# Optimization experiments

Hardware: AMD Instinct MI355X
Metric: run time of the kernel (lower is better)

The kernel has to match this reference:

```python
import jax, jax.numpy as jnp
import numpy as np

DIM = 256; HEADS = 4; HD = DIM // HEADS; SCALE = HD ** -0.5
CBS = 4; CSTRIDE = 2; SBS = 4; NSEL = 16; WS = 7
B = 4; H = 64; W = 64


def _unfold(x, bs, stride):
    # x: (B,H,W,C) -> (B, nh*nw, C*bs*bs), flat channel order matches torch F.unfold
    # (index = c*bs*bs + kh*bs + kw)
    b, h, w, c = x.shape
    nh = (h - bs) // stride + 1
    nw = (w - bs) // stride + 1
    cols = [x[:, kh:kh + nh * stride:stride, kw:kw + nw * stride:stride, :]
            for kh in range(bs) for kw in range(bs)]
    p = jnp.stack(cols, axis=-1)  # (B,nh,nw,C,bs*bs)
    return p.reshape(b, nh * nw, c * bs * bs)


def _rel_pos_index(ws):
    coords = np.stack(np.meshgrid(np.arange(ws), np.arange(ws), indexing='ij')).reshape(2, -1)
    rel = (coords[:, :, None] - coords[:, None, :]).transpose(1, 2, 0).copy()
    rel[:, :, 0] += ws - 1
    rel[:, :, 1] += ws - 1
    rel[:, :, 0] *= 2 * ws - 1
    return jnp.asarray(rel.sum(-1))  # (ws*ws, ws*ws) int


def _mlp(x, w1, b1, w2, b2):
    return jax.nn.gelu(x @ w1 + b1, approximate=False) @ w2 + b2


def _window_attn(x, qkv_w, qkv_b, proj_w, proj_b, bias_table):
    b, c, h, w = x.shape
    ws = WS
    ph = (ws - h % ws) % ws
    pw = (ws - w % ws) % ws
    xp = jnp.pad(x, ((0, 0), (0, 0), (0, ph), (0, pw)))
    hp, wp = h + ph, w + pw
    xw = xp.reshape(b, c, hp // ws, ws, wp // ws, ws).transpose(0, 2, 4, 3, 5, 1).reshape(-1, ws * ws, c)
    bw = xw.shape[0]
    qkv = (xw @ qkv_w + qkv_b).reshape(bw, ws * ws, 3, HEADS, HD).transpose(2, 0, 3, 1, 4)
    q, k, v = qkv[0], qkv[1], qkv[2]
    attn = jnp.einsum('bhnd,bhmd->bhnm', q, k) * SCALE
    rpi = _rel_pos_index(ws)
    bias = bias_table[rpi.reshape(-1)].reshape(ws * ws, ws * ws, HEADS).transpose(2, 0, 1)
    attn = jax.nn.softmax(attn + bias[None], axis=-1)
    o = jnp.einsum('bhnm,bhmd->bhnd', attn, v).transpose(0, 2, 1, 3).reshape(bw, ws * ws, c)
    o = o @ proj_w + proj_b
    o = o.reshape(b, hp // ws, wp // ws, ws, ws, c).transpose(0, 5, 1, 3, 2, 4).reshape(b, c, hp, wp)
    return o[:, :, :h, :w]


def _forward(x, qkv_cmp_w, qkv_cmp_b, qkv_slc_w, qkv_slc_b,
             cmpk_w1, cmpk_b1, cmpk_w2, cmpk_b2,
             cmpv_w1, cmpv_b1, cmpv_w2, cmpv_b2, pos_embed,
             win_qkv_w, win_qkv_b, win_proj_w, win_proj_b, win_bias_table,
             proj_cmp_w, proj_cmp_b, proj_slc_w, proj_slc_b,
             gate_w1, gate_b1, gate_w2, gate_b2):
    b, c, h, w = x.shape
    n = h * w
    xs = x.reshape(b, c, n).transpose(0, 2, 1)  # (B,N,C)

    # --- compressed branch ---
    qkv = (xs @ qkv_cmp_w + qkv_cmp_b).reshape(b, n, 3, HEADS, HD).transpose(2, 0, 3, 1, 4)
    q_c, k_c, v_c = qkv[0], qkv[1], qkv[2]  # (B,heads,N,hd)
    k_flat = k_c.transpose(0, 2, 1, 3).reshape(b, n, c)
    v_flat = v_c.transpose(0, 2, 1, 3).reshape(b, n, c)
    fk = _unfold(k_flat.reshape(b, h, w, c), CBS, CSTRIDE)  # (B,nb,C*16)
    fv = _unfold(v_flat.reshape(b, h, w, c), CBS, CSTRIDE)
    nb = fk.shape[1]
    # replicate torch's reshape of the channel-major unfold vector into (bs*bs, dim)
    kpos = (fk.reshape(b, nb, CBS * CBS, c) + pos_embed[None]).reshape(b, nb, CBS * CBS * c)
    k_cmp = _mlp(kpos, cmpk_w1, cmpk_b1, cmpk_w2, cmpk_b2)  # (B,nb,C)
    v_cmp = _mlp(fv, cmpv_w1, cmpv_b1, cmpv_w2, cmpv_b2)
    kch = k_cmp.reshape(b, nb, HEADS, HD).transpose(0, 2, 1, 3)
    vch = v_cmp.reshape(b, nb, HEADS, HD).transpose(0, 2, 1, 3)
    attn_cmp = jax.nn.softmax(jnp.einsum('bhnd,bhmd->bhnm', q_c, kch) * SCALE, axis=-1)
    out_cmp = jnp.einsum('bhnm,bhmd->bhnd', attn_cmp, vch).transpose(0, 2, 1, 3).reshape(b, n, c)
    out_cmp = out_cmp @ proj_cmp_w + proj_cmp_b

    # --- selected branch ---
    qkv2 = (xs @ qkv_slc_w + qkv_slc_b).reshape(b, n, 3, HEADS, HD).transpose(2, 0, 3, 1, 4)
    q_s, k_s, v_s = qkv2[0], qkv2[1], qkv2[2]
    ks_flat = k_s.transpose(0, 2, 1, 3).reshape(b, n, c)
    vs_flat = v_s.transpose(0, 2, 1, 3).reshape(b, n, c)
    imp = attn_cmp.sum(axis=1).mean(axis=1)  # (B, nb)
    ns = min(NSEL, nb)
    _, idx = jax.lax.top_k(imp, ns)
    fkb = _unfold(ks_flat.reshape(b, h, w, c), SBS, SBS)
    fvb = _unfold(vs_flat.reshape(b, h, w, c), SBS, SBS)
    nb2 = fkb.shape[1]
    kb = fkb.reshape(b, nb2, SBS * SBS, c)
    vb = fvb.reshape(b, nb2, SBS * SBS, c)
    idx = jnp.clip(idx, 0, nb2 - 1)
    k_slc = jnp.take_along_axis(kb, idx[:, :, None, None], axis=1).reshape(b, ns * SBS * SBS, c)
    v_slc = jnp.take_along_axis(vb, idx[:, :, None, None], axis=1).reshape(b, ns * SBS * SBS, c)
    ksh = k_slc.reshape(b, -1, HEADS, HD).transpose(0, 2, 1, 3)
    vsh = v_slc.reshape(b, -1, HEADS, HD).transpose(0, 2, 1, 3)
    attn_slc = jax.nn.softmax(jnp.einsum('bhnd,bhmd->bhnm', q_s, ksh) * SCALE, axis=-1)
    out_slc = jnp.einsum('bhnm,bhmd->bhnd', attn_slc, vsh).transpose(0, 2, 1, 3).reshape(b, n, c)
    out_slc = out_slc @ proj_slc_w + proj_slc_b

    # --- window branch ---
    out_win = _window_attn(x, win_qkv_w, win_qkv_b, win_proj_w, win_proj_b, win_bias_table)
    out_win = out_win.reshape(b, c, n).transpose(0, 2, 1)

    # --- gated combination ---
    g = jax.nn.sigmoid(jax.nn.gelu(xs @ gate_w1 + gate_b1, approximate=False) @ gate_w2 + gate_b2)
    out = g[..., 0:1] * out_cmp + g[..., 1:2] * out_slc + g[..., 2:3] * out_win
    return out.transpose(0, 2, 1).reshape(b, c, h, w)


def setup_inputs() -> dict:
    key = jax.random.key(0)
    ks = jax.random.split(key, 16)
    s = 0.02
    d = {
        'x': jax.random.normal(ks[0], (B, DIM, H, W), jnp.float32),
        'qkv_cmp_w': jax.random.normal(ks[1], (DIM, 3 * DIM)) * s,
        'qkv_cmp_b': jnp.zeros((3 * DIM,)),
        'qkv_slc_w': jax.random.normal(ks[2], (DIM, 3 * DIM)) * s,
        'qkv_slc_b': jnp.zeros((3 * DIM,)),
        'cmpk_w1': jax.random.normal(ks[3], (DIM * CBS * CBS, 2 * DIM)) * s,
        'cmpk_b1': jnp.zeros((2 * DIM,)),
        'cmpk_w2': jax.random.normal(ks[4], (2 * DIM, DIM)) * s,
        'cmpk_b2': jnp.zeros((DIM,)),
        'cmpv_w1': jax.random.normal(ks[5], (DIM * CBS * CBS, 2 * DIM)) * s,
        'cmpv_b1': jnp.zeros((2 * DIM,)),
        'cmpv_w2': jax.random.normal(ks[6], (2 * DIM, DIM)) * s,
        'cmpv_b2': jnp.zeros((DIM,)),
        'pos_embed': jax.random.normal(ks[7], (1, CBS * CBS, DIM)) * s,
        'win_qkv_w': jax.random.normal(ks[8], (DIM, 3 * DIM)) * s,
        'win_qkv_b': jnp.zeros((3 * DIM,)),
        'win_proj_w': jax.random.normal(ks[9], (DIM, DIM)) * s,
        'win_proj_b': jnp.zeros((DIM,)),
        'win_bias_table': jax.random.normal(ks[10], ((2 * WS - 1) ** 2, HEADS)) * s,
        'proj_cmp_w': jax.random.normal(ks[11], (DIM, DIM)) * s,
        'proj_cmp_b': jnp.zeros((DIM,)),
        'proj_slc_w': jax.random.normal(ks[12], (DIM, DIM)) * s,
        'proj_slc_b': jnp.zeros((DIM,)),
        'gate_w1': jax.random.normal(ks[13], (DIM, DIM // 4)) * s,
        'gate_b1': jnp.zeros((DIM // 4,)),
        'gate_w2': jax.random.normal(ks[14], (DIM // 4, 3)) * s,
        'gate_b2': jnp.zeros((3,)),
    }
    return d


def reference(x, qkv_cmp_w, qkv_cmp_b, qkv_slc_w, qkv_slc_b,
              cmpk_w1, cmpk_b1, cmpk_w2, cmpk_b2,
              cmpv_w1, cmpv_b1, cmpv_w2, cmpv_b2, pos_embed,
              win_qkv_w, win_qkv_b, win_proj_w, win_proj_b, win_bias_table,
              proj_cmp_w, proj_cmp_b, proj_slc_w, proj_slc_b,
              gate_w1, gate_b1, gate_w2, gate_b2):
    return _forward(x, qkv_cmp_w, qkv_cmp_b, qkv_slc_w, qkv_slc_b,
                    cmpk_w1, cmpk_b1, cmpk_w2, cmpk_b2,
                    cmpv_w1, cmpv_b1, cmpv_w2, cmpv_b2, pos_embed,
                    win_qkv_w, win_qkv_b, win_proj_w, win_proj_b, win_bias_table,
                    proj_cmp_w, proj_cmp_b, proj_slc_w, proj_slc_b,
                    gate_w1, gate_b1, gate_w2, gate_b2)
```

## Files before the change

kernel.cpp:

```cpp
#include <hip/hip_runtime.h>
#include <stdint.h>
#include <stddef.h>


#define DEV __device__ __forceinline__

typedef __attribute__((ext_vector_type(8))) short short8;
typedef __attribute__((ext_vector_type(4))) float f32x4;
typedef unsigned short u16;

DEV u16 f2bf(float f){
    unsigned u = __float_as_uint(f);
    u += 0x7FFFu + ((u>>16)&1u);
    return (u16)(u>>16);
}
DEV float bf2f(u16 u){ return __uint_as_float(((unsigned)u)<<16); }

#define LGKM0() asm volatile("s_waitcnt lgkmcnt(0)" ::: "memory")

__global__ void k_xs(const float* __restrict__ x, u16* __restrict__ xh,
                     u16* __restrict__ xl){
    __shared__ float t[32][33];
    int b = blockIdx.z; int c0 = blockIdx.y*32; int n0 = blockIdx.x*32;
    int tx = threadIdx.x, ty = threadIdx.y;
    for(int i=ty;i<32;i+=8)
        t[i][tx] = x[((size_t)(b*256 + c0+i))*4096 + n0 + tx];
    __syncthreads();
    for(int i=ty;i<32;i+=8){
        float v = t[tx][i];
        u16 h = f2bf(v);
        size_t o = ((size_t)(b*4096 + n0+i))*256 + c0 + tx;
        xh[o] = h;
        xl[o] = f2bf(v - bf2f(h));
    }
}

__global__ void k_wt(const float* __restrict__ W, u16* __restrict__ WT,
                     int K, int N){
    __shared__ float t[32][33];
    int k0 = blockIdx.x*32, n0 = blockIdx.y*32;
    int tx = threadIdx.x, ty = threadIdx.y;
    for(int i=ty;i<32;i+=8)
        if(k0+i<K && n0+tx<N) t[i][tx] = W[(size_t)(k0+i)*N + n0+tx];
    __syncthreads();
    for(int i=ty;i<32;i+=8)
        if(n0+i<N && k0+tx<K) WT[(size_t)(n0+i)*K + k0+tx] = f2bf(t[tx][i]);
}

__global__ void k_wt2(const float* __restrict__ W, u16* __restrict__ Hi,
                      u16* __restrict__ Lo, int K, int N){
    __shared__ float t[32][33];
    int k0 = blockIdx.x*32, n0 = blockIdx.y*32;
    int tx = threadIdx.x, ty = threadIdx.y;
    for(int i=ty;i<32;i+=8)
        if(k0+i<K && n0+tx<N) t[i][tx] = W[(size_t)(k0+i)*N + n0+tx];
    __syncthreads();
    for(int i=ty;i<32;i+=8)
        if(n0+i<N && k0+tx<K){
            float v = t[tx][i];
            u16 h = f2bf(v);
            Hi[(size_t)(n0+i)*K + k0+tx] = h;
            Lo[(size_t)(n0+i)*K + k0+tx] = f2bf(v - bf2f(h));
        }
}

__global__ void k_vt(const float* __restrict__ vc, u16* __restrict__ vt,
                     int NK, int ldk){
    __shared__ float t[32][33];
    int b = blockIdx.z; int k0 = blockIdx.x*32; int c0 = blockIdx.y*32;
    int tx = threadIdx.x, ty = threadIdx.y;
    for(int i=ty;i<32;i+=8){
        int k = k0+i;
        t[i][tx] = (k < NK) ? vc[((size_t)(b*NK + k))*256 + c0 + tx] : 0.f;
    }
    __syncthreads();
    for(int i=ty;i<32;i+=8){
        int k = k0+tx;
        if(k < ldk)
            vt[((size_t)(b*256 + c0+i))*ldk + k] = f2bf(t[tx][i]);
    }
}

__global__ __launch_bounds__(256) void k_gemm(
        const float* __restrict__ A, const float* __restrict__ W,
        const float* __restrict__ bias, float* __restrict__ C,
        int M, int K, int Nn, int act)
{
    __shared__ float As[16][68];
    __shared__ float Bs[16][64];
    const int m0 = blockIdx.y*64, n0 = blockIdx.x*64;
    const int t = threadIdx.x, tx = t&15, ty = t>>4;
    float acc[4][4] = {};
    const int am = t>>2;
    const int ak = (t&3)*4;
    const bool arow_ok = (m0+am) < M;

    for(int k0=0;k0<K;k0+=16){
        float4 av = make_float4(0.f,0.f,0.f,0.f);
        if(arow_ok) av = *reinterpret_cast<const float4*>(&A[(size_t)(m0+am)*K + k0 + ak]);
        As[ak+0][am]=av.x; As[ak+1][am]=av.y; As[ak+2][am]=av.z; As[ak+3][am]=av.w;
        {
            int n = t&63, kb = t>>6;
            #pragma unroll
            for(int r=0;r<4;r++){
                int kk = r*4 + kb; float v = 0.f;
                if(n0+n < Nn) v = W[(size_t)(k0+kk)*Nn + n0+n];
                Bs[kk][n] = v;
            }
        }
        __syncthreads();
        #pragma unroll
        for(int kk=0;kk<16;kk++){
            float a0=As[kk][ty*4+0], a1=As[kk][ty*4+1], a2=As[kk][ty*4+2], a3=As[kk][ty*4+3];
            float b0=Bs[kk][tx*4+0], b1=Bs[kk][tx*4+1], b2=Bs[kk][tx*4+2], b3=Bs[kk][tx*4+3];
            acc[0][0]=fmaf(a0,b0,acc[0][0]); acc[0][1]=fmaf(a0,b1,acc[0][1]);
            acc[0][2]=fmaf(a0,b2,acc[0][2]); acc[0][3]=fmaf(a0,b3,acc[0][3]);
            acc[1][0]=fmaf(a1,b0,acc[1][0]); acc[1][1]=fmaf(a1,b1,acc[1][1]);
            acc[1][2]=fmaf(a1,b2,acc[1][2]); acc[1][3]=fmaf(a1,b3,acc[1][3]);
            acc[2][0]=fmaf(a2,b0,acc[2][0]); acc[2][1]=fmaf(a2,b1,acc[2][1]);
            acc[2][2]=fmaf(a2,b2,acc[2][2]); acc[2][3]=fmaf(a2,b3,acc[2][3]);
            acc[3][0]=fmaf(a3,b0,acc[3][0]); acc[3][1]=fmaf(a3,b1,acc[3][1]);
            acc[3][2]=fmaf(a3,b2,acc[3][2]); acc[3][3]=fmaf(a3,b3,acc[3][3]);
        }
        __syncthreads();
    }
    #pragma unroll
    for(int i=0;i<4;i++){
        int m = m0 + ty*4 + i;
        if(m >= M) continue;
        #pragma unroll
        for(int j=0;j<4;j++){
            int n = n0 + tx*4 + j;
            if(n >= Nn) continue;
            float v = acc[i][j] + (bias ? bias[n] : 0.f);
            if(act==1)      v = 0.5f*v*(1.0f + erff(v*0.70710678118654752f));
            else if(act==2) v = 1.0f/(1.0f + expf(-v));
            C[(size_t)m*Nn + n] = v;
        }
    }
}

template<int WM, int WN, int AM, int BMD, int NSPLIT, int OBF>
__global__ __launch_bounds__(256) void k_mgs(
        const float* __restrict__ Af, const u16* __restrict__ Ah,
        const u16* __restrict__ Al,
        const float* __restrict__ Bf, const u16* __restrict__ Bh,
// ... 87 lines not shown
                        h[j] = (short)hb;
                        if(SP) l[j] = (short)f2bf(vv[j] - bf2f(hb));
                    }
                } else {
                    if(lok){
                        h = *reinterpret_cast<const short8*>(Bh + (size_t)(n0+brow)*ldb + kt + e);
                        if(SP && BMD==2)
                            l = *reinterpret_cast<const short8*>(Bl + (size_t)(n0+brow)*ldb + kt + e);
                    }
                }
                int byteoff = brow*128 + (colbyte ^ ((brow&7)<<4));
                *reinterpret_cast<short8*>(reinterpret_cast<char*>(Bhi)+byteoff) = h;
                if(SP)
                    *reinterpret_cast<short8*>(reinterpret_cast<char*>(Blo)+byteoff) = l;
            }
        }
        __syncthreads();
        __builtin_amdgcn_s_setprio(1);
        #pragma unroll
        for(int kb=0;kb<2;kb++){
            short8 ah[WM], al[WM], bh[WN], bl[WN];
            #pragma unroll
            for(int i=0;i<WM;i++){
                int ar = wm + i*16 + (lane&15);
                int ab = ar*128 + (((kb*64) + ((lane>>4)*16)) ^ ((ar&7)<<4));
                ah[i] = *reinterpret_cast<const short8*>(reinterpret_cast<const char*>(Ahi)+ab);
                if(SP)
                    al[i] = *reinterpret_cast<const short8*>(reinterpret_cast<const char*>(Alo)+ab);
            }
            #pragma unroll
            for(int i=0;i<WN;i++){
                int br = wn + i*16 + (lane&15);
                int bb = br*128 + (((kb*64) + ((lane>>4)*16)) ^ ((br&7)<<4));
                bh[i] = *reinterpret_cast<const short8*>(reinterpret_cast<const char*>(Bhi)+bb);
                if(SP)
                    bl[i] = *reinterpret_cast<const short8*>(reinterpret_cast<const char*>(Blo)+bb);
            }
            #pragma unroll
            for(int mi=0;mi<WM;mi++)
                #pragma unroll
                for(int ni=0;ni<WN;ni++){
                    if(SP){
                        acc[mi][ni] = __builtin_amdgcn_mfma_f32_16x16x32_bf16(
                                          al[mi], bh[ni], acc[mi][ni], 0, 0, 0);
                        acc[mi][ni] = __builtin_amdgcn_mfma_f32_16x16x32_bf16(
                                          ah[mi], bl[ni], acc[mi][ni], 0, 0, 0);
                    }
                    acc[mi][ni] = __builtin_amdgcn_mfma_f32_16x16x32_bf16(
                                      ah[mi], bh[ni], acc[mi][ni], 0, 0, 0);
                }
        }
        __builtin_amdgcn_s_setprio(0);
        __syncthreads();
    }
    #pragma unroll
    for(int mi=0;mi<WM;mi++){
        #pragma unroll
        for(int ni=0;ni<WN;ni++){
            int col = n0 + wn + ni*16 + (lane&15);
            if(col >= N) continue;
            int rowb = m0 + wm + mi*16 + ((lane>>4)*4);
            float bv = bias ? bias[col] : 0.f;
            #pragma unroll
            for(int r=0;r<4;r++){
                int m = rowb + r;
                if(m >= M) continue;
                float v = acc[mi][ni][r]*scale + bv;
                if(act==1)      v = 0.5f*v*(1.0f + erff(v*0.70710678118654752f));
                else if(act==2) v = 1.0f/(1.0f + expf(-v));
                if(OBF==2){
                    u16 hb = f2bf(v);
                    Cb [(size_t)m*ldc + col] = hb;
                    Cb2[(size_t)m*ldc + col] = f2bf(v - bf2f(hb));
                } else if(OBF==1){
                    Cb[(size_t)m*ldc + col] = f2bf(v);
                } else {
                    C [(size_t)m*ldc + col] = v;
                }
            }
        }
    }
}

template<int SPLIT, int IMP, int ONEPASS, int NKR, int NT, int LDV>
__global__ __launch_bounds__(256) void k_fattn(
    const float* __restrict__ Qg, const u16* __restrict__ Khg,
    const u16* __restrict__ Klg, const u16* __restrict__ VTg,
    u16* __restrict__ Og, float* __restrict__ impp)
{
    const int qb = blockIdx.x, h = blockIdx.y, b = blockIdx.z;
    const int tid = threadIdx.x, lane = tid&63, wv = tid>>6;
    const int wm = wv*16;
    const int rgrp = lane>>4;
    const int cidx = lane&15;

    __shared__ u16 Qh[64*64];
    __shared__ u16 Ql[SPLIT?64*64:8];
    __shared__ u16 Kh[64*64];
    __shared__ u16 Kl[SPLIT?64*64:8];
    __shared__ u16 Pl[64*64];
    __shared__ u16 Vl[64*64];
    __shared__ float part[4][64];
    __shared__ float colacc[IMP? NT*64 : 8];

    const int srow = tid>>2;
    const int scol0 = (tid&3)*32;

    short8 kh_r[2], kl_r[2], v_r[2];

    auto LK = [&](int t){
        const bool ok = (t*64 + srow) < NKR;
        const u16* srch = &Khg[((size_t)b*NKR + t*64 + srow)*256 + h*64];
        const u16* srcl = SPLIT ? &Klg[((size_t)b*NKR + t*64 + srow)*256 + h*64] : nullptr;
        #pragma unroll
        for(int c=0;c<2;c++){
            int e = (scol0 + c*16)>>1;
            short8 hh = {}, ll = {};
            if(ok){
                hh = *reinterpret_cast<const short8*>(srch+e);
                if(SPLIT) ll = *reinterpret_cast<const short8*>(srcl+e);
            }
            kh_r[c] = hh;
            if(SPLIT) kl_r[c] = ll;
        }
    };
    auto WK = [&](){
        #pragma unroll
        for(int c=0;c<2;c++){
            int colbyte = scol0 + c*16;
            int byteoff = srow*128 + (colbyte ^ ((srow&7)<<4));
            *reinterpret_cast<short8*>(reinterpret_cast<char*>(Kh)+byteoff) = kh_r[c];
            if(SPLIT)
                *reinterpret_cast<short8*>(reinterpret_cast<char*>(Kl)+byteoff) = kl_r[c];
        }
    };
    auto LV = [&](int t){
        const u16* src = &VTg[((size_t)b*256 + h*64 + srow)*LDV + t*64];
        #pragma unroll
        for(int c=0;c<2;c++){
            int e = (scol0 + c*16)>>1;
            short8 hh = {};
            if(t*64 + e + 8 <= LDV)
                hh = *reinterpret_cast<const short8*>(src + e);
            v_r[c] = hh;
        }
    };
    auto WV = [&](){
        #pragma unroll
        for(int c=0;c<2;c++){
            int colbyte = scol0 + c*16;
            int byteoff = srow*128 + (colbyte ^ ((srow&7)<<4));
            *reinterpret_cast<short8*>(reinterpret_cast<char*>(Vl)+byteoff) = v_r[c];
        }
    };

    {
        const float* src = &Qg[((size_t)b*4096 + qb*64 + srow)*768 + h*64];
        #pragma unroll
        for(int c=0;c<2;c++){
            int colbyte = scol0 + c*16;
            int e = colbyte>>1;
            float4 v0 = *reinterpret_cast<const float4*>(src+e);
            float4 v1 = *reinterpret_cast<const float4*>(src+e+4);
            float vv[8]={v0.x,v0.y,v0.z,v0.w,v1.x,v1.y,v1.z,v1.w};
            short8 hh, ll;
            #pragma unroll
// ... 96 lines not shown
                    acc[ni] = __builtin_amdgcn_mfma_f32_16x16x32_bf16(ah, bl, acc[ni], 0,0,0);
                }
                acc[ni] = __builtin_amdgcn_mfma_f32_16x16x32_bf16(ah, bh, acc[ni], 0,0,0);
            }
        }
        __builtin_amdgcn_s_setprio(0);
        float cs[4] = {0.f,0.f,0.f,0.f};
        #pragma unroll
        for(int ni=0;ni<4;ni++){
            #pragma unroll
            for(int r=0;r<4;r++){
                int col = kt + ni*16 + cidx;
                float p = 0.f;
                if(col < NKR){
                    p = __expf(acc[ni][r]*0.125f);
                    if(!ONEPASS) p *= inv[r];
                    else lsum[r] += p;
                }
                int prow = wm + rgrp*4 + r;
                int pcol = ni*16 + cidx;
                int byteoff = prow*128 + ((pcol*2) ^ ((prow&7)<<4));
                *reinterpret_cast<u16*>(reinterpret_cast<char*>(Pl)+byteoff) = f2bf(p);
                if(IMP) cs[ni] += p;
            }
        }
        if(IMP){
            #pragma unroll
            for(int ni=0;ni<4;ni++){
                cs[ni] += __shfl_xor(cs[ni],16);
                cs[ni] += __shfl_xor(cs[ni],32);
            }
            if(rgrp==0){
                #pragma unroll
                for(int ni=0;ni<4;ni++)
                    part[wv][ni*16+cidx] = cs[ni];
            }
        }
        LGKM0();
        __builtin_amdgcn_s_barrier();
        if(IMP && tid < 64)
            colacc[kt+tid] += ((part[0][tid]+part[1][tid])+part[2][tid])+part[3][tid];
        __builtin_amdgcn_s_setprio(1);
        #pragma unroll
        for(int kb=0;kb<2;kb++){
            int koff = kb*64 + rgrp*16;
            int ar = wm + cidx;
            int ab = ar*128 + (koff ^ ((ar&7)<<4));
            short8 pa = *reinterpret_cast<const short8*>(reinterpret_cast<const char*>(Pl)+ab);
            #pragma unroll
            for(int ni=0;ni<4;ni++){
                int br = ni*16 + cidx;
                int bb = br*128 + (koff ^ ((br&7)<<4));
                short8 vb = *reinterpret_cast<const short8*>(reinterpret_cast<const char*>(Vl)+bb);
                acc_o[ni] = __builtin_amdgcn_mfma_f32_16x16x32_bf16(pa, vb, acc_o[ni], 0,0,0);
            }
        }
        __builtin_amdgcn_s_setprio(0);
    }
    if(ONEPASS){
        #pragma unroll
        for(int r=0;r<4;r++){
            float l = lsum[r];
            l += __shfl_xor(l,1); l += __shfl_xor(l,2);
            l += __shfl_xor(l,4); l += __shfl_xor(l,8);
            inv[r] = 1.f/l;
        }
    }
    __syncthreads();
    #pragma unroll
    for(int ni=0;ni<4;ni++){
        #pragma unroll
        for(int r=0;r<4;r++){
            int q = qb*64 + wm + rgrp*4 + r;
            int d = ni*16 + cidx;
            float o = acc_o[ni][r];
            if(ONEPASS) o *= inv[r];
            Og[((size_t)b*4096 + q)*256 + h*64 + d] = f2bf(o);
        }
    }
    if(IMP){
        size_t base = ((size_t)((b*4+h)*64) + qb)*976;
        for(int k=tid; k<NT*64 && k<976; k+=256)
            impp[base+k] = colacc[k];
    }
}

__global__ void k_unfold2(const float* __restrict__ qkv, const float* __restrict__ pos,
                          u16* __restrict__ kh, u16* __restrict__ kl,
                          u16* __restrict__ vv){
    int row = blockIdx.x;
    int b = row / 961, blk = row % 961;
    int bi = blk / 31, bj = blk % 31;
    for(int j = threadIdx.x; j < 4096; j += 256){
        int ch = j >> 4;
        int khh = (j >> 2) & 3, kw = j & 3;
        int n = (bi*2 + khh)*64 + (bj*2 + kw);
        size_t base = ((size_t)(b*4096) + n)*768 + ch;
        float kv = qkv[base + 256] + pos[j];
        float va = qkv[base + 512];
        u16 h = f2bf(kv);
        kh[(size_t)row*4096 + j] = h;
        kl[(size_t)row*4096 + j] = f2bf(kv - bf2f(h));
        vv[(size_t)row*4096 + j] = f2bf(va);
    }
}

__global__ void k_imp_reduce(const float* __restrict__ impp, float* __restrict__ imp){
    __shared__ float part[4][64];
    int b = blockIdx.y;
    int k = blockIdx.x*64 + (threadIdx.x & 63);
    int rr = threadIdx.x >> 6;
    float s = 0.f;
    if(k < 976){
        for(int r=rr; r<256; r+=4)
            s += impp[((size_t)(b*256) + r)*976 + k];
    }
    part[rr][threadIdx.x & 63] = s;
    __syncthreads();
    if(threadIdx.x < 64 && k < 961){
        float t = ((part[0][threadIdx.x] + part[1][threadIdx.x])
                 + part[2][threadIdx.x]) + part[3][threadIdx.x];
        imp[b*961 + k] = t;
    }
}

__global__ __launch_bounds__(256) void k_topk(const float* __restrict__ imp,
                                              int* __restrict__ idx){
    int b = blockIdx.x;
    __shared__ float v[961];
    __shared__ float wvv[4];
    __shared__ int   wvi[4];
    int t = threadIdx.x;
    int lane = t & 63, wid = t >> 6;
    for(int i=t;i<961;i+=256) v[i] = imp[b*961+i];
    __syncthreads();
    for(int it=0; it<16; it++){
        float bv = -1e30f; int bi = 1<<30;
        for(int i=t;i<961;i+=256){
            float val = v[i];
            if(val > bv){ bv=val; bi=i; }
        }
        #pragma unroll
        for(int off=32; off>0; off>>=1){
            float ov = __shfl_xor(bv, off);
            int   oi = __shfl_xor(bi, off);
            if(ov > bv || (ov == bv && oi < bi)){ bv = ov; bi = oi; }
        }
        if(lane==0){ wvv[wid]=bv; wvi[wid]=bi; }
        __syncthreads();
        if(t==0){
            float gb=wvv[0]; int gi=wvi[0];
            #pragma unroll
            for(int w=1;w<4;w++){
                if(wvv[w]>gb || (wvv[w]==gb && wvi[w]<gi)){ gb=wvv[w]; gi=wvi[w]; }
            }
            idx[b*16+it] = gi;
            v[gi] = -1e30f;
        }
        __syncthreads();
    }
}

__global__ void k_gather_sel(const float* __restrict__ qkv2, const int* __restrict__ idx,
                             u16* __restrict__ Ks, float* __restrict__ Vs){
    int row = blockIdx.x;
    int b = row >> 8, tt = row & 255;
    int sel = tt >> 4, p = tt & 15;
    int blk = idx[b*16+sel]; if(blk > 255) blk = 255;
    int bi = blk >> 4, bj = blk & 15;
    int cc = threadIdx.x;
    int y = bi*4 + ((cc>>2)&3), xx = bj*4 + (cc&3);
    int ch = p*16 + (cc>>4);
    size_t src = ((size_t)(b*4096) + y*64 + xx)*768;
    Ks[(size_t)row*256 + cc] = f2bf(qkv2[src + 256 + ch]);
    Vs[(size_t)row*256 + cc] = qkv2[src + 512 + ch];
}

__global__ void k_xw(const u16* __restrict__ xh, u16* __restrict__ xw){
    int row = blockIdx.x;
    int wb = row / 49, t = row % 49;
    int b = wb / 100, wrem = wb % 100;
    int wy = wrem / 10, wx = wrem % 10;
    int ty = t / 7, tx = t % 7;
    int y = wy*7 + ty, xx = wx*7 + tx;
    int c = threadIdx.x;
    u16 v = 0;
// ... 45 lines not shown
        for(int d=0;d<64;d++){
            float a0=0,a1=0;
            for(int j=0;j<48;j+=2){
                a0 = fmaf(ls[lane][j],   lv[j][d],   a0);
                a1 = fmaf(ls[lane][j+1], lv[j+1][d], a1);
            }
            a0 = fmaf(ls[lane][48], lv[48][d], a0);
            op[d] = f2bf((a0+a1)*inv);
        }
    }
}

__global__ void k_combine(const float* __restrict__ ocp, const float* __restrict__ osp,
                          const float* __restrict__ owp, const float* __restrict__ g,
                          float* __restrict__ out){
    __shared__ float tile[32][33];
    int b = blockIdx.z; int c0 = blockIdx.y*32, n0 = blockIdx.x*32;
    int tx = threadIdx.x, ty = threadIdx.y;
    for(int i=ty;i<32;i+=8){
        int n = n0 + i;
        float g0 = g[(size_t)(b*4096+n)*3 + 0];
        float g1 = g[(size_t)(b*4096+n)*3 + 1];
        float g2 = g[(size_t)(b*4096+n)*3 + 2];
        int y = n >> 6, xx = n & 63;
        int wy = y/7, ty2 = y%7, wx = xx/7, tx2 = xx%7;
        size_t wrow = (size_t)(b*100 + wy*10 + wx)*49 + ty2*7 + tx2;
        size_t base = ((size_t)(b*4096) + n)*256 + c0;
        float vc = ocp[base + tx];
        float vs = osp[base + tx];
        float vw = owp[wrow*256 + c0 + tx];
        tile[i][tx] = g0*vc + g1*vs + g2*vw;
    }
    __syncthreads();
    for(int i=ty;i<32;i+=8)
        out[((size_t)(b*256 + c0+i))*4096 + n0 + tx] = tile[tx][i];
}

extern "C" void kernel_launch(void* const* d_in, const int* in_sizes, int n_in,
                              void* d_out, int out_size, void* d_ws, size_t ws_size,
                              hipStream_t stream)
{
    typedef const float* fp;
    fp x          = (fp)d_in[0];
    fp qkv_cmp_w  = (fp)d_in[1];  fp qkv_cmp_b = (fp)d_in[2];
    fp qkv_slc_w  = (fp)d_in[3];  fp qkv_slc_b = (fp)d_in[4];
    fp cmpk_w1    = (fp)d_in[5];  fp cmpk_b1   = (fp)d_in[6];
    fp cmpk_w2    = (fp)d_in[7];  fp cmpk_b2   = (fp)d_in[8];
    fp cmpv_w1    = (fp)d_in[9];  fp cmpv_b1   = (fp)d_in[10];
    fp cmpv_w2    = (fp)d_in[11]; fp cmpv_b2   = (fp)d_in[12];
    fp pos_embed  = (fp)d_in[13];
    fp win_qkv_w  = (fp)d_in[14]; fp win_qkv_b = (fp)d_in[15];
    fp win_proj_w = (fp)d_in[16]; fp win_proj_b= (fp)d_in[17];
    fp win_btab   = (fp)d_in[18];
    fp proj_cmp_w = (fp)d_in[19]; fp proj_cmp_b= (fp)d_in[20];
    fp proj_slc_w = (fp)d_in[21]; fp proj_slc_b= (fp)d_in[22];
    fp gate_w1    = (fp)d_in[23]; fp gate_b1   = (fp)d_in[24];
    fp gate_w2    = (fp)d_in[25]; fp gate_b2   = (fp)d_in[26];
    (void)in_sizes; (void)n_in; (void)out_size;

    char* ws = (char*)d_ws;
    size_t off = 0;
    auto alloc = [&](size_t bytes)->size_t{
        size_t r = off; off += (bytes + 255) & ~(size_t)255; return r;
    };
    const size_t XSH  = alloc((size_t)16384*256*2);
    const size_t XSL  = alloc((size_t)16384*256*2);
    const size_t QKV  = alloc((size_t)16384*768*4);
    const size_t BIGA = alloc((size_t)4*4096*976*4);
    const size_t HID  = alloc((size_t)3844*512*4);
    const size_t KCH  = alloc((size_t)3844*256*2);
    const size_t KCL  = alloc((size_t)3844*256*2);
    const size_t VC   = alloc((size_t)3844*256*4);
    const size_t S_IMPP = (size_t)4096*976*4;
    const size_t S_OC   = (size_t)16384*256*4;
    const size_t S_PB   = (size_t)4*4096*976*2;
    const size_t POOL = alloc(S_IMPP + S_OC + S_OC + S_PB);
    const size_t IMP  = alloc((size_t)4*961*4);
    const size_t IDX  = alloc((size_t)4*16*4);
    const size_t KS   = alloc((size_t)4*256*256*2);
    const size_t VS   = alloc((size_t)4*256*256*4);
    const size_t G2   = alloc((size_t)16384*3*4);
    const size_t VTC  = alloc((size_t)4*256*976*2);
    const size_t VTS  = alloc((size_t)4*256*256*2);
    const size_t TQS  = alloc((size_t)768*256*2);
    const size_t TWQ  = alloc((size_t)768*256*2);
    const size_t TV1  = alloc((size_t)512*4096*2);
    const size_t TV2  = alloc((size_t)256*512*2);
    const size_t TPC  = alloc((size_t)256*256*2);
    const size_t TPS  = alloc((size_t)256*256*2);
    const size_t TWP  = alloc((size_t)256*256*2);
    const size_t TG1  = alloc((size_t)64*256*2);
    const size_t TQCH = alloc((size_t)768*256*2);
    const size_t TQCL = alloc((size_t)768*256*2);
    const size_t TK1H = alloc((size_t)512*4096*2);
    const size_t TK1L = alloc((size_t)512*4096*2);
    const size_t TK2H = alloc((size_t)256*512*2);
    const size_t TK2L = alloc((size_t)256*512*2);
    if(off > ws_size) return;

    u16*   p_xsh = (u16*)(ws + XSH);
    u16*   p_xsl = (u16*)(ws + XSL);
    float* p_qkv = (float*)(ws + QKV);
    u16*   p_bigb= (u16*)  (ws + BIGA);
    u16*   p_uv  = (u16*)  (ws + BIGA);
    float* p_oslc= (float*)(ws + BIGA);
    float* p_owp = (float*)(ws + BIGA + 20971520);
    float* p_hid = (float*)(ws + HID);
    u16*   p_kch = (u16*)(ws + KCH);
    u16*   p_kcl = (u16*)(ws + KCL);
    float* p_vc  = (float*)(ws + VC);
    float* p_impp= (float*)(ws + POOL);
    u16*   p_oc16= (u16*)  (ws + POOL + S_IMPP);
    float* p_ocp = (float*)(ws + POOL + S_IMPP + S_OC);
    u16*   p_ukh = (u16*)  (ws + POOL);
    u16*   p_ukl = p_ukh + (size_t)3844*4096;
    u16*   p_xwb = (u16*)  (ws + POOL);
    u16*   p_owin= (u16*)  (ws + POOL + S_IMPP);
    float* p_imp = (float*)(ws + IMP);
    int*   p_idx = (int*)  (ws + IDX);
    u16*   p_ks  = (u16*)(ws + KS);
    float* p_vs  = (float*)(ws + VS);
    float* p_g   = (float*)(ws + G2);
    u16*   p_vtc = (u16*)(ws + VTC);
    u16*   p_vts = (u16*)(ws + VTS);
    u16* t_qs = (u16*)(ws + TQS);
    u16* t_wq = (u16*)(ws + TWQ);
    u16* t_v1 = (u16*)(ws + TV1);
    u16* t_v2 = (u16*)(ws + TV2);
    u16* t_pc = (u16*)(ws + TPC);
    u16* t_ps = (u16*)(ws + TPS);
    u16* t_wp = (u16*)(ws + TWP);
    u16* t_g1 = (u16*)(ws + TG1);
    u16* t_qch= (u16*)(ws + TQCH);
    u16* t_qcl= (u16*)(ws + TQCL);
    u16* t_k1h= (u16*)(ws + TK1H);
    u16* t_k1l= (u16*)(ws + TK1L);
    u16* t_k2h= (u16*)(ws + TK2H);
    u16* t_k2l= (u16*)(ws + TK2L);

    auto wt = [&](fp W, u16* WT, int K, int Nn){
        k_wt<<<dim3((K+31)/32, (Nn+31)/32), dim3(32,8), 0, stream>>>(W, WT, K, Nn);
    };
    auto wt2 = [&](fp W, u16* H, u16* L, int K, int Nn){
        k_wt2<<<dim3((K+31)/32, (Nn+31)/32), dim3(32,8), 0, stream>>>(W, H, L, K, Nn);
    };

    wt(qkv_slc_w, t_qs, 256, 768);
    wt(win_qkv_w, t_wq, 256, 768);
    wt(cmpv_w1,   t_v1, 4096, 512);
    wt(cmpv_w2,   t_v2, 512, 256);
    wt(proj_cmp_w,t_pc, 256, 256);
    wt(proj_slc_w,t_ps, 256, 256);
    wt(win_proj_w,t_wp, 256, 256);
    wt(gate_w1,   t_g1, 256, 64);
    wt2(qkv_cmp_w, t_qch, t_qcl, 256, 768);
    wt2(cmpk_w1,   t_k1h, t_k1l, 4096, 512);
    wt2(cmpk_w2,   t_k2h, t_k2l, 512, 256);

    k_xs<<<dim3(128,8,4), dim3(32,8), 0, stream>>>(x, p_xsh, p_xsl);
    k_mgs<4,4,2,2,3,0><<<dim3(6,128), 256, 0, stream>>>(
        nullptr, p_xsh, p_xsl, nullptr, t_qch, t_qcl, qkv_cmp_b, p_qkv, nullptr, nullptr,
        16384, 768, 256, 256, 256, 768, 0, 1.0f, 0, 0, 0);
    k_unfold2<<<3844, 256, 0, stream>>>(p_qkv, pos_embed, p_ukh, p_ukl, p_uv);
    k_mgs<2,2,2,2,3,0><<<dim3(8,61), 256, 0, stream>>>(
        nullptr, p_ukh, p_ukl, nullptr, t_k1h, t_k1l, cmpk_b1, p_hid, nullptr, nullptr,
        3844, 512, 4096, 4096, 4096, 512, 1, 1.0f, 0, 0, 0);
    k_mgs<2,2,0,2,3,2><<<dim3(4,61), 256, 0, stream>>>(
        p_hid, nullptr, nullptr, nullptr, t_k2h, t_k2l, cmpk_b2, nullptr, p_kch, p_kcl,
        3844, 256, 512, 512, 512, 256, 0, 1.0f, 0, 0, 0);
    k_mgs<2,2,1,1,1,0><<<dim3(8,61), 256, 0, stream>>>(
        nullptr, p_uv, nullptr, nullptr, t_v1, nullptr, cmpv_b1, p_hid, nullptr, nullptr,
        3844, 512, 4096, 4096, 4096, 512, 1, 1.0f, 0, 0, 0);
    k_mgs<2,2,0,1,1,0><<<dim3(4,61), 256, 0, stream>>>(
        p_hid, nullptr, nullptr, nullptr, t_v2, nullptr, cmpv_b2, p_vc, nullptr, nullptr,
        3844, 256, 512, 512, 512, 256, 0, 1.0f, 0, 0, 0);
    k_vt<<<dim3(31,8,4), dim3(32,8), 0, stream>>>(p_vc, p_vtc, 961, 976);
    k_fattn<1,1,0,961,16,976><<<dim3(64,4,4), 256, 0, stream>>>(
        p_qkv, p_kch, p_kcl, p_vtc, p_oc16, p_impp);
    k_imp_reduce<<<dim3(16,4), 256, 0, stream>>>(p_impp, p_imp);
    k_topk<<<4, 256, 0, stream>>>(p_imp, p_idx);
    k_mgs<4,4,1,1,1,0><<<dim3(2,128), 256, 0, stream>>>(
        nullptr, p_oc16, nullptr, nullptr, t_pc, nullptr, proj_cmp_b, p_ocp, nullptr, nullptr,
        16384, 256, 256, 256, 256, 256, 0, 1.0f, 0, 0, 0);
    k_mgs<4,4,1,1,1,0><<<dim3(6,128), 256, 0, stream>>>(
        nullptr, p_xsh, nullptr, nullptr, t_qs, nullptr, qkv_slc_b, p_qkv, nullptr, nullptr,
        16384, 768, 256, 256, 256, 768, 0, 1.0f, 0, 0, 0);
    k_xw<<<19600, 256, 0, stream>>>(p_xsh, p_xwb);
    k_mgs<4,4,1,1,1,1><<<dim3(6,154), 256, 0, stream>>>(
        nullptr, p_xwb, nullptr, nullptr, t_wq, nullptr, win_qkv_b, nullptr, p_bigb, nullptr,
        19600, 768, 256, 256, 256, 768, 0, 1.0f, 0, 0, 0);
    k_attn_win<<<dim3(400,4), 64, 0, stream>>>(p_bigb, win_btab, p_owin);
    k_mgs<4,4,1,1,1,0><<<dim3(2,154), 256, 0, stream>>>(
        nullptr, p_owin, nullptr, nullptr, t_wp, nullptr, win_proj_b, p_owp, nullptr, nullptr,
        19600, 256, 256, 256, 256, 256, 0, 1.0f, 0, 0, 0);
    k_gather_sel<<<1024, 256, 0, stream>>>(p_qkv, p_idx, p_ks, p_vs);
    k_vt<<<dim3(8,8,4), dim3(32,8), 0, stream>>>(p_vs, p_vts, 256, 256);
    k_fattn<0,0,1,256,4,256><<<dim3(64,4,4), 256, 0, stream>>>(
        p_qkv, p_ks, nullptr, p_vts, p_oc16, nullptr);
    k_mgs<4,4,1,1,1,0><<<dim3(2,128), 256, 0, stream>>>(
        nullptr, p_oc16, nullptr, nullptr, t_ps, nullptr, proj_slc_b, p_oslc, nullptr, nullptr,
        16384, 256, 256, 256, 256, 256, 0, 1.0f, 0, 0, 0);
    k_mgs<2,2,1,1,1,0><<<dim3(1,256), 256, 0, stream>>>(
        nullptr, p_xsh, nullptr, nullptr, t_g1, nullptr, gate_b1, p_hid, nullptr, nullptr,
        16384, 64, 256, 256, 256, 64, 1, 1.0f, 0, 0, 0);
    k_gemm<<<dim3(1,256), 256, 0, stream>>>(p_hid, gate_w2, gate_b2, p_g,
                                            16384, 64, 3, 2);
    k_combine<<<dim3(128,8,4), dim3(32,8), 0, stream>>>(p_ocp, p_oslc, p_owp, p_g,
                                                        (float*)d_out);
}
```

Before: 794.0 us.

## Fuse unfold into compressor GEMM loads and fold pos_embed into bias

Drops the materialized unfold buffers, which held about 3844x4096 hi/lo/v bf16 values. The compressor MLP GEMMs now gather their A tiles straight from per-token K/V arrays, using a permuted K ordering in the transposed weights so each 64-wide k-tile is one contiguous channel span of a single patch position. The pos_embed addition is moved into the first-layer bias as pos@W1+b1, computed once by a small kernel. This removes a large write-then-read of the unfolded data. In exchange the A loads are strided gathers, and pos_embed is no longer split into hi/lo parts inside the K path, which slightly changes the rounding.

```diff
diff --git a/kernel.cpp b/kernel.cpp
--- a/kernel.cpp
+++ b/kernel.cpp
@@ -36,19 +36,7 @@
 }
 
 __global__ void k_wt(const float* __restrict__ W, u16* __restrict__ WT,
-                     int K, int N){
-    __shared__ float t[32][33];
-    int k0 = blockIdx.x*32, n0 = blockIdx.y*32;
-    int tx = threadIdx.x, ty = threadIdx.y;
-    for(int i=ty;i<32;i+=8)
-        if(k0+i<K && n0+tx<N) t[i][tx] = W[(size_t)(k0+i)*N + n0+tx];
-    __syncthreads();
-    for(int i=ty;i<32;i+=8)
-        if(n0+i<N && k0+tx<K) WT[(size_t)(n0+i)*K + k0+tx] = f2bf(t[tx][i]);
-}
-
-__global__ void k_wt2(const float* __restrict__ W, u16* __restrict__ Hi,
-                      u16* __restrict__ Lo, int K, int N){
+                     int K, int N, int perm){
     __shared__ float t[32][33];
     int k0 = blockIdx.x*32, n0 = blockIdx.y*32;
     int tx = threadIdx.x, ty = threadIdx.y;
@@ -57,11 +45,55 @@
     __syncthreads();
     for(int i=ty;i<32;i+=8)
         if(n0+i<N && k0+tx<K){
+            int k = k0+tx;
+            int kd = perm ? (((k&15)<<8)|(k>>4)) : k;
+            WT[(size_t)(n0+i)*K + kd] = f2bf(t[tx][i]);
+        }
+}
+
+__global__ void k_wt2(const float* __restrict__ W, u16* __restrict__ Hi,
+                      u16* __restrict__ Lo, int K, int N, int perm){
+    __shared__ float t[32][33];
+    int k0 = blockIdx.x*32, n0 = blockIdx.y*32;
+    int tx = threadIdx.x, ty = threadIdx.y;
+    for(int i=ty;i<32;i+=8)
+        if(k0+i<K && n0+tx<N) t[i][tx] = W[(size_t)(k0+i)*N + n0+tx];
+    __syncthreads();
+    for(int i=ty;i<32;i+=8)
+        if(n0+i<N && k0+tx<K){
+            int k = k0+tx;
+            int kd = perm ? (((k&15)<<8)|(k>>4)) : k;
             float v = t[tx][i];
             u16 h = f2bf(v);
-            Hi[(size_t)(n0+i)*K + k0+tx] = h;
-            Lo[(size_t)(n0+i)*K + k0+tx] = f2bf(v - bf2f(h));
-        }
+            Hi[(size_t)(n0+i)*K + kd] = h;
+            Lo[(size_t)(n0+i)*K + kd] = f2bf(v - bf2f(h));
+        }
+}
+
+__global__ void k_splitkv(const float* __restrict__ qkv, u16* __restrict__ kh,
+                          u16* __restrict__ kl, u16* __restrict__ vf){
+    int n = blockIdx.x, b = blockIdx.y, c = threadIdx.x;
+    size_t src = ((size_t)(b*4096) + n)*768 + c;
+    size_t dst = ((size_t)(b*4096) + n)*256 + c;
+    float kv = qkv[src + 256];
+    u16 h = f2bf(kv);
+    kh[dst] = h;
+    kl[dst] = f2bf(kv - bf2f(h));
+    vf[dst] = f2bf(qkv[src + 512]);
+}
+
+__global__ void k_posw1(const float* __restrict__ pos, const float* __restrict__ W1,
+                        const float* __restrict__ b1, float* __restrict__ out){
+    __shared__ float part[4][64];
+    int tn = threadIdx.x & 63, r = threadIdx.x >> 6;
+    int n = blockIdx.x*64 + tn;
+    float s = 0.f;
+    for(int j=r; j<4096; j+=4)
+        s += pos[j] * W1[(size_t)j*512 + n];
+    part[r][tn] = s;
+    __syncthreads();
+    if(threadIdx.x < 64)
+        out[n] = b1[n] + (((part[0][tn]+part[1][tn])+part[2][tn])+part[3][tn]);
 }
 
 __global__ void k_vt(const float* __restrict__ vc, u16* __restrict__ vt,
@@ -315,6 +347,130 @@
     }
 }
 
+template<int SPLIT>
+__global__ __launch_bounds__(256) void k_mgs_unf(
+        const u16* __restrict__ Fh, const u16* __restrict__ Fl,
+        const u16* __restrict__ Bh, const u16* __restrict__ Bl,
+        const float* __restrict__ bias, float* __restrict__ C)
+{
+    constexpr int M = 3844, N = 512, K = 4096;
+    __shared__ u16 Ahi[64*64];
+    __shared__ u16 Alo[SPLIT ? 64*64 : 8];
+    __shared__ u16 Bhi[64*64];
+    __shared__ u16 Blo[SPLIT ? 64*64 : 8];
+
+    const int m0 = blockIdx.y*64, n0 = blockIdx.x*64;
+    const int tid = threadIdx.x, lane = tid&63, wv = tid>>6;
+    const int wm = (wv>>1)*32, wn = (wv&1)*32;
+    f32x4 acc[2][2] = {};
+
+    const int arow = tid >> 2;
+    const int acol0 = (tid & 3) * 32;
+    const int m = m0 + arow;
+    const bool ok = m < M;
+    const int mm = ok ? m : 0;
+    const int b  = mm / 961;
+    const int blk = mm % 961;
+    const int bi = blk / 31, bj = blk % 31;
+    const u16* fbase_h = Fh + (size_t)b*4096*256;
+    const u16* fbase_l = SPLIT ? (Fl + (size_t)b*4096*256) : nullptr;
+
+    for(int kt=0; kt<K; kt+=64){
+        {
+            int sub = kt >> 8;
+            int kh = sub >> 2, kw = sub & 3;
+            int n = (bi*2 + kh)*64 + (bj*2 + kw);
+            size_t srcoff = (size_t)n*256 + (kt & 255);
+            #pragma unroll
+            for(int c=0;c<2;c++){
+                int colbyte = acol0 + c*16;
+                int e = colbyte >> 1;
+                short8 h = {}, l = {};
+                if(ok){
+                    h = *reinterpret_cast<const short8*>(fbase_h + srcoff + e);
+                    if(SPLIT)
+                        l = *reinterpret_cast<const short8*>(fbase_l + srcoff + e);
+                }
+                int byteoff = arow*128 + (colbyte ^ ((arow&7)<<4));
+                *reinterpret_cast<short8*>(reinterpret_cast<char*>(Ahi)+byteoff) = h;
+                if(SPLIT)
+                    *reinterpret_cast<short8*>(reinterpret_cast<char*>(Alo)+byteoff) = l;
+            }
+        }
+        {
+            int brow = tid >> 2;
+            int bcol0 = (tid & 3) * 32;
+            #pragma unroll
+            for(int c=0;c<2;c++){
+                int colbyte = bcol0 + c*16;
+                int e = colbyte >> 1;
+                short8 h = *reinterpret_cast<const short8*>(Bh + (size_t)(n0+brow)*K + kt + e);
+                short8 l = {};
+                if(SPLIT)
+                    l = *reinterpret_cast<const short8*>(Bl + (size_t)(n0+brow)*K + kt + e);
+                int byteoff = brow*128 + (colbyte ^ ((brow&7)<<4));
+                *reinterpret_cast<short8*>(reinterpret_cast<char*>(Bhi)+byteoff) = h;
+                if(SPLIT)
+                    *reinterpret_cast<short8*>(reinterpret_cast<char*>(Blo)+byteoff) = l;
+            }
+        }
+        __syncthreads();
+        __builtin_amdgcn_s_setprio(1);
+        #pragma unroll
+        for(int kb=0;kb<2;kb++){
+            short8 ah[2], al[2], bh[2], bl[2];
+            #pragma unroll
+            for(int i=0;i<2;i++){
+                int ar = wm + i*16 + (lane&15);
+                int ab = ar*128 + (((kb*64) + ((lane>>4)*16)) ^ ((ar&7)<<4));
+                ah[i] = *reinterpret_cast<const short8*>(reinterpret_cast<const char*>(Ahi)+ab);
+                if(SPLIT)
+                    al[i] = *reinterpret_cast<const short8*>(reinterpret_cast<const char*>(Alo)+ab);
+            }
+            #pragma unroll
+            for(int i=0;i<2;i++){
+                int br = wn + i*16 + (lane&15);
+                int bb = br*128 + (((kb*64) + ((lane>>4)*16)) ^ ((br&7)<<4));
+                bh[i] = *reinterpret_cast<const short8*>(reinterpret_cast<const char*>(Bhi)+bb);
+                if(SPLIT)
+                    bl[i] = *reinterpret_cast<const short8*>(reinterpret_cast<const char*>(Blo)+bb);
+            }
+            #pragma unroll
+            for(int mi=0;mi<2;mi++)
+                #pragma unroll
+                for(int ni=0;ni<2;ni++){
+                    if(SPLIT){
+                        acc[mi][ni] = __builtin_amdgcn_mfma_f32_16x16x32_bf16(
+                                          al[mi], bh[ni], acc[mi][ni], 0, 0, 0);
+                        acc[mi][ni] = __builtin_amdgcn_mfma_f32_16x16x32_bf16(
+                                          ah[mi], bl[ni], acc[mi][ni], 0, 0, 0);
+                    }
+                    acc[mi][ni] = __builtin_amdgcn_mfma_f32_16x16x32_bf16(
+                                      ah[mi], bh[ni], acc[mi][ni], 0, 0, 0);
+                }
+        }
+        __builtin_amdgcn_s_setprio(0);
+        __syncthreads();
+    }
+    #pragma unroll
+    for(int mi=0;mi<2;mi++){
+        #pragma unroll
+        for(int ni=0;ni<2;ni++){
+            int col = n0 + wn + ni*16 + (lane&15);
+            int rowb = m0 + wm + mi*16 + ((lane>>4)*4);
+            float bv = bias[col];
+            #pragma unroll
+            for(int r=0;r<4;r++){
+                int mr = rowb + r;
+                if(mr >= M) continue;
+                float v = acc[mi][ni][r] + bv;
+                v = 0.5f*v*(1.0f + erff(v*0.70710678118654752f));
+                C[(size_t)mr*512 + col] = v;
+            }
+        }
+    }
+}
+
 template<int SPLIT, int IMP, int ONEPASS, int NKR, int NT, int LDV>
 __global__ __launch_bounds__(256) void k_fattn(
     const float* __restrict__ Qg, const u16* __restrict__ Khg,
@@ -577,26 +733,6 @@
         size_t base = ((size_t)((b*4+h)*64) + qb)*976;
         for(int k=tid; k<NT*64 && k<976; k+=256)
             impp[base+k] = colacc[k];
-    }
-}
-
-__global__ void k_unfold2(const float* __restrict__ qkv, const float* __restrict__ pos,
-                          u16* __restrict__ kh, u16* __restrict__ kl,
-                          u16* __restrict__ vv){
-    int row = blockIdx.x;
-    int b = row / 961, blk = row % 961;
-    int bi = blk / 31, bj = blk % 31;
-    for(int j = threadIdx.x; j < 4096; j += 256){
-        int ch = j >> 4;
-        int khh = (j >> 2) & 3, kw = j & 3;
-        int n = (bi*2 + khh)*64 + (bj*2 + kw);
-        size_t base = ((size_t)(b*4096) + n)*768 + ch;
-        float kv = qkv[base + 256] + pos[j];
-        float va = qkv[base + 512];
-        u16 h = f2bf(kv);
-        kh[(size_t)row*4096 + j] = h;
-        kl[(size_t)row*4096 + j] = f2bf(kv - bf2f(h));
-        vv[(size_t)row*4096 + j] = f2bf(va);
     }
 }
 
@@ -808,6 +944,7 @@
     const size_t G2   = alloc((size_t)16384*3*4);
     const size_t VTC  = alloc((size_t)4*256*976*2);
     const size_t VTS  = alloc((size_t)4*256*256*2);
+    const size_t POSB = alloc((size_t)512*4);
     const size_t TQS  = alloc((size_t)768*256*2);
     const size_t TWQ  = alloc((size_t)768*256*2);
     const size_t TV1  = alloc((size_t)512*4096*2);
@@ -828,7 +965,6 @@
     u16*   p_xsl = (u16*)(ws + XSL);
     float* p_qkv = (float*)(ws + QKV);
     u16*   p_bigb= (u16*)  (ws + BIGA);
-    u16*   p_uv  = (u16*)  (ws + BIGA);
     float* p_oslc= (float*)(ws + BIGA);
     float* p_owp = (float*)(ws + BIGA + 20971520);
     float* p_hid = (float*)(ws + HID);
@@ -838,8 +974,9 @@
     float* p_impp= (float*)(ws + POOL);
     u16*   p_oc16= (u16*)  (ws + POOL + S_IMPP);
     float* p_ocp = (float*)(ws + POOL + S_IMPP + S_OC);
-    u16*   p_ukh = (u16*)  (ws + POOL);
-    u16*   p_ukl = p_ukh + (size_t)3844*4096;
+    u16*   p_kfh = (u16*)  (ws + POOL);
+    u16*   p_kfl = p_kfh + (size_t)4*4096*256;
+    u16*   p_vf  = p_kfl + (size_t)4*4096*256;
     u16*   p_xwb = (u16*)  (ws + POOL);
     u16*   p_owin= (u16*)  (ws + POOL + S_IMPP);
     float* p_imp = (float*)(ws + IMP);
@@ -849,6 +986,7 @@
     float* p_g   = (float*)(ws + G2);
     u16*   p_vtc = (u16*)(ws + VTC);
     u16*   p_vts = (u16*)(ws + VTS);
+    float* p_posb= (float*)(ws + POSB);
     u16* t_qs = (u16*)(ws + TQS);
     u16* t_wq = (u16*)(ws + TWQ);
     u16* t_v1 = (u16*)(ws + TV1);
@@ -864,39 +1002,38 @@
     u16* t_k2h= (u16*)(ws + TK2H);
     u16* t_k2l= (u16*)(ws + TK2L);
 
-    auto wt = [&](fp W, u16* WT, int K, int Nn){
-        k_wt<<<dim3((K+31)/32, (Nn+31)/32), dim3(32,8), 0, stream>>>(W, WT, K, Nn);
+    auto wt = [&](fp W, u16* WT, int K, int Nn, int perm){
+        k_wt<<<dim3((K+31)/32, (Nn+31)/32), dim3(32,8), 0, stream>>>(W, WT, K, Nn, perm);
     };
-    auto wt2 = [&](fp W, u16* H, u16* L, int K, int Nn){
-        k_wt2<<<dim3((K+31)/32, (Nn+31)/32), dim3(32,8), 0, stream>>>(W, H, L, K, Nn);
+    auto wt2 = [&](fp W, u16* H, u16* L, int K, int Nn, int perm){
+        k_wt2<<<dim3((K+31)/32, (Nn+31)/32), dim3(32,8), 0, stream>>>(W, H, L, K, Nn, perm);
     };
 
-    wt(qkv_slc_w, t_qs, 256, 768);
-    wt(win_qkv_w, t_wq, 256, 768);
-    wt(cmpv_w1,   t_v1, 4096, 512);
-    wt(cmpv_w2,   t_v2, 512, 256);
-    wt(proj_cmp_w,t_pc, 256, 256);
-    wt(proj_slc_w,t_ps, 256, 256);
-    wt(win_proj_w,t_wp, 256, 256);
-    wt(gate_w1,   t_g1, 256, 64);
-    wt2(qkv_cmp_w, t_qch, t_qcl, 256, 768);
-    wt2(cmpk_w1,   t_k1h, t_k1l, 4096, 512);
-    wt2(cmpk_w2,   t_k2h, t_k2l, 512, 256);
+    wt(qkv_slc_w, t_qs, 256, 768, 0);
+    wt(win_qkv_w, t_wq, 256, 768, 0);
+    wt(cmpv_w1,   t_v1, 4096, 512, 1);
+    wt(cmpv_w2,   t_v2, 512, 256, 0);
+    wt(proj_cmp_w,t_pc, 256, 256, 0);
+    wt(proj_slc_w,t_ps, 256, 256, 0);
+    wt(win_proj_w,t_wp, 256, 256, 0);
+    wt(gate_w1,   t_g1, 256, 64, 0);
+    wt2(qkv_cmp_w, t_qch, t_qcl, 256, 768, 0);
+    wt2(cmpk_w1,   t_k1h, t_k1l, 4096, 512, 1);
+    wt2(cmpk_w2,   t_k2h, t_k2l, 512, 256, 0);
+    k_posw1<<<8, 256, 0, stream>>>(pos_embed, cmpk_w1, cmpk_b1, p_posb);
 
     k_xs<<<dim3(128,8,4), dim3(32,8), 0, stream>>>(x, p_xsh, p_xsl);
     k_mgs<4,4,2,2,3,0><<<dim3(6,128), 256, 0, stream>>>(
         nullptr, p_xsh, p_xsl, nullptr, t_qch, t_qcl, qkv_cmp_b, p_qkv, nullptr, nullptr,
         16384, 768, 256, 256, 256, 768, 0, 1.0f, 0, 0, 0);
-    k_unfold2<<<3844, 256, 0, stream>>>(p_qkv, pos_embed, p_ukh, p_ukl, p_uv);
-    k_mgs<2,2,2,2,3,0><<<dim3(8,61), 256, 0, stream>>>(
-        nullptr, p_ukh, p_ukl, nullptr, t_k1h, t_k1l, cmpk_b1, p_hid, nullptr, nullptr,
-        3844, 512, 4096, 4096, 4096, 512, 1, 1.0f, 0, 0, 0);
+    k_splitkv<<<dim3(4096,4), 256, 0, stream>>>(p_qkv, p_kfh, p_kfl, p_vf);
+    k_mgs_unf<1><<<dim3(8,61), 256, 0, stream>>>(
+        p_kfh, p_kfl, t_k1h, t_k1l, p_posb, p_hid);
     k_mgs<2,2,0,2,3,2><<<dim3(4,61), 256, 0, stream>>>(
         p_hid, nullptr, nullptr, nullptr, t_k2h, t_k2l, cmpk_b2, nullptr, p_kch, p_kcl,
         3844, 256, 512, 512, 512, 256, 0, 1.0f, 0, 0, 0);
-    k_mgs<2,2,1,1,1,0><<<dim3(8,61), 256, 0, stream>>>(
-        nullptr, p_uv, nullptr, nullptr, t_v1, nullptr, cmpv_b1, p_hid, nullptr, nullptr,
-        3844, 512, 4096, 4096, 4096, 512, 1, 1.0f, 0, 0, 0);
+    k_mgs_unf<0><<<dim3(8,61), 256, 0, stream>>>(
+        p_vf, nullptr, t_v1, nullptr, cmpv_b1, p_hid);
     k_mgs<2,2,0,1,1,0><<<dim3(4,61), 256, 0, stream>>>(
         p_hid, nullptr, nullptr, nullptr, t_v2, nullptr, cmpv_b2, p_vc, nullptr, nullptr,
         3844, 256, 512, 512, 512, 256, 0, 1.0f, 0, 0, 0);
```

Result: slower. 992.5 us (+25.0%).
